# Kernel tuning notes

Hardware: AMD Instinct MI355X
Metric: run time of the kernel (lower is better)

The kernel has to match this reference:

```python
import jax, jax.numpy as jnp
import numpy as np

L = 3          # num_layers
D = 512        # hidden_dim
B, N = 8, 1024
EPS = 1e-5


def layernorm(x, gamma, beta):
    mu = jnp.mean(x, axis=-1, keepdims=True)
    var = jnp.var(x, axis=-1, keepdims=True)
    return (x - mu) * jax.lax.rsqrt(var + EPS) * gamma + beta


def setup_inputs() -> dict:
    key = jax.random.key(0)
    ks = jax.random.split(key, 12)
    s = 1.0 / np.sqrt(D)
    node_features = jax.random.normal(ks[0], (B, N, D), dtype=jnp.float32)
    adjacency_matrix = jax.random.randint(ks[1], (B, N, N), 0, 2, dtype=jnp.int32)
    return {
        "node_features": node_features,
        "adjacency_matrix": adjacency_matrix,
        # attn_linear: Linear(2D, 1) -> weight [2D], bias scalar, per layer
        "attn_w": jax.random.normal(ks[2], (L, 2 * D), dtype=jnp.float32) * (1.0 / np.sqrt(2 * D)),
        "attn_b": jax.random.normal(ks[3], (L,), dtype=jnp.float32) * 0.01,
        "W1": jax.random.normal(ks[4], (L, D, 4 * D), dtype=jnp.float32) * s,
        "b1": jnp.zeros((L, 4 * D), dtype=jnp.float32),
        "W2": jax.random.normal(ks[5], (L, 4 * D, D), dtype=jnp.float32) * (1.0 / np.sqrt(4 * D)),
        "b2": jnp.zeros((L, D), dtype=jnp.float32),
        "g1": jnp.ones((L, D), dtype=jnp.float32),
        "beta1": jnp.zeros((L, D), dtype=jnp.float32),
        "g2": jnp.ones((L, D), dtype=jnp.float32),
        "beta2": jnp.zeros((L, D), dtype=jnp.float32),
    }


def reference(node_features, adjacency_matrix, attn_w, attn_b, W1, b1, W2, b2, g1, beta1, g2, beta2):
    n = adjacency_matrix.shape[-1]
    # adjacency + self loops; mask of allowed edges
    mask = (adjacency_matrix.astype(jnp.float32) + jnp.eye(n, dtype=jnp.float32)) > 0  # [B,N,N]
    x = node_features
    d = x.shape[-1]
    for l in range(attn_w.shape[0]):
        # score_ij = a1.h_i + a2.h_j + b  (== Linear(concat(h_i,h_j)))
        si = x @ attn_w[l, :d]           # [B,N]
        sj = x @ attn_w[l, d:]           # [B,N]
        scores = si[:, :, None] + sj[:, None, :] + attn_b[l]   # [B,N,N]
        scores = jnp.where(scores >= 0, scores, 0.2 * scores)  # LeakyReLU(0.2)
        scores = jnp.where(mask, scores, -jnp.inf)
        attn = jax.nn.softmax(scores, axis=-1)                  # diag always unmasked
        agg = jnp.einsum('bij,bjd->bid', attn, x)
        h = layernorm(x + agg, g1[l], beta1[l])
        ff = jax.nn.gelu(h @ W1[l] + b1[l], approximate=False) @ W2[l] + b2[l]
        x = layernorm(h + ff, g2[l], beta2[l])
    return x
```

## Files before the change

### kernel.cpp

```cpp
#include <hip/hip_runtime.h>
#include <math.h>

#define NB 8
#define NN 1024
#define DD 512

typedef unsigned short u16;
typedef unsigned int u32;
typedef unsigned long long u64;
typedef __attribute__((ext_vector_type(8))) short bfrag;
typedef __attribute__((ext_vector_type(4))) float ffrag;

__device__ __forceinline__ u16 f2b(float f) {
    union { float f; u32 u; } v; v.f = f;
    u32 r = v.u + 0x7fffu + ((v.u >> 16) & 1u);
    return (u16)(r >> 16);
}
__device__ __forceinline__ float b2f(u16 b) {
    union { u32 u; float f; } v; v.u = ((u32)b) << 16;
    return v.f;
}

__device__ __forceinline__ float gelu_cheap(float v) {
    float s = v * 0.70710678118654752f;
    float a = fabsf(s);
    float t = 1.0f / (1.0f + 0.3275911f * a);
    float p = ((((1.061405429f * t - 1.453152027f) * t + 1.421413741f) * t
                - 0.284496736f) * t + 0.254829592f) * t;
    float erfa = 1.0f - p * __expf(-a * a);
    float erfs = copysignf(erfa, s);
    return 0.5f * v * (1.0f + erfs);
}

__device__ __forceinline__ void gload_lds16(const void* g, void* l) {
    __builtin_amdgcn_global_load_lds(
        (const __attribute__((address_space(1))) void*)g,
        (__attribute__((address_space(3))) void*)l, 16, 0, 0);
}

__global__ __launch_bounds__(256) void mask_pack(const int* __restrict__ adj,
                                                 u64* __restrict__ mb) {
    int idx = blockIdx.x * 256 + threadIdx.x;
    int w = idx & 15;
    int bi = idx >> 4;
    int i = bi & 1023;
    const int4* p = (const int4*)(adj + (size_t)bi * NN + w * 64);
    u64 m = 0;
#pragma unroll
    for (int q = 0; q < 16; ++q) {
        int4 v = p[q];
        if (v.x > 0) m |= 1ull << (q * 4 + 0);
        if (v.y > 0) m |= 1ull << (q * 4 + 1);
        if (v.z > 0) m |= 1ull << (q * 4 + 2);
        if (v.w > 0) m |= 1ull << (q * 4 + 3);
    }
    if (w == (i >> 6)) m |= 1ull << (i & 63);
    mb[idx] = m;
}

__global__ __launch_bounds__(256) void transpose_cvt(
    const float* __restrict__ in, u16* __restrict__ out,
    int R, int C, size_t inStr, size_t outStr)
{
    __shared__ float tile[32][33];
    int z = blockIdx.z;
    int r0 = blockIdx.y * 32, c0 = blockIdx.x * 32;
    int t = threadIdx.x;
    int tr = t >> 3, tc = (t & 7) * 4;
    float4 v = *(const float4*)(in + inStr * z + (size_t)(r0 + tr) * C + c0 + tc);
    tile[tr][tc + 0] = v.x; tile[tr][tc + 1] = v.y;
    tile[tr][tc + 2] = v.z; tile[tr][tc + 3] = v.w;
    __syncthreads();
    u32 w0 = (u32)f2b(tile[tc + 0][tr]) | ((u32)f2b(tile[tc + 1][tr]) << 16);
    u32 w1 = (u32)f2b(tile[tc + 2][tr]) | ((u32)f2b(tile[tc + 3][tr]) << 16);
    uint2 wv; wv.x = w0; wv.y = w1;
    *(uint2*)(out + outStr * z + (size_t)(c0 + tr) * R + r0 + tc) = wv;
}

__global__ __launch_bounds__(256) void score_proj_kernel(
    const float* __restrict__ x, const float* __restrict__ w,
    float* __restrict__ si, float* __restrict__ sj)
{
    int wave = threadIdx.x >> 6;
    int lane = threadIdx.x & 63;
    int row = blockIdx.x * 4 + wave;
    const float4* xr = (const float4*)(x + (size_t)row * DD) + lane * 2;
    const float4* w1 = (const float4*)(w) + lane * 2;
    const float4* w2 = (const float4*)(w + DD) + lane * 2;
    float a = 0.f, b2 = 0.f;
#pragma unroll
    for (int c = 0; c < 2; ++c) {
        float4 xv = xr[c], wa = w1[c], wb = w2[c];
        a  += xv.x * wa.x + xv.y * wa.y + xv.z * wa.z + xv.w * wa.w;
        b2 += xv.x * wb.x + xv.y * wb.y + xv.z * wb.z + xv.w * wb.w;
    }
#pragma unroll
    for (int off = 32; off > 0; off >>= 1) {
        a  += __shfl_xor(a, off);
        b2 += __shfl_xor(b2, off);
    }
    if (lane == 0) { si[row] = a; sj[row] = b2; }
}

__global__ __launch_bounds__(256) void softmax_p(
    const float* __restrict__ si, const float* __restrict__ sj,
    const float* __restrict__ attn_b, const u64* __restrict__ mb,
    u16* __restrict__ P)
{
    __shared__ u16 sb[8 * NN];
    int b  = blockIdx.x >> 7;
    int i0 = (blockIdx.x & 127) * 8;
    int tid = threadIdx.x;
    int r = tid >> 5, l32 = tid & 31;
    int i = i0 + r;
    float bb = attn_b[0];
    float siv = si[b * NN + i];
    const float* sjb = sj + b * NN;
    const u64* mbr = mb + ((size_t)b * NN + i) * 16;

    float sv[32];
    float mx = -INFINITY;
#pragma unroll
    for (int q = 0; q < 32; ++q) {
        int j = q * 32 + l32;
        u64 w = mbr[q >> 1];
        int bit = ((q & 1) << 5) + l32;
        float s = siv + sjb[j] + bb;
        s = (s >= 0.f) ? s : 0.2f * s;
        s = ((w >> bit) & 1ull) ? s : -INFINITY;
        sv[q] = s;
        mx = fmaxf(mx, s);
    }
#pragma unroll
    for (int off = 16; off > 0; off >>= 1) mx = fmaxf(mx, __shfl_xor(mx, off, 32));
    float sum = 0.f;
#pragma unroll
    for (int q = 0; q < 32; ++q) {
        float p = __expf(sv[q] - mx);
        sv[q] = p;
        sum += p;
    }
#pragma unroll
    for (int off = 16; off > 0; off >>= 1) sum += __shfl_xor(sum, off, 32);
    float inv = 1.f / sum;
#pragma unroll
    for (int q = 0; q < 32; ++q)
        sb[r * NN + q * 32 + l32] = f2b(sv[q] * inv);
    __syncthreads();
    const uint4* src = (const uint4*)sb;
    uint4* dst = (uint4*)(P + ((size_t)b * NN + i0) * NN);
#pragma unroll
    for (int t = 0; t < 4; ++t) dst[t * 256 + tid] = src[t * 256 + tid];
}

template <int EPI>
__global__ __launch_bounds__(256) void gemm64(
    const u16* __restrict__ A, const u16* __restrict__ Bm,
    const float* __restrict__ bias, const void* __restrict__ res,
    void* __restrict__ Cout, int K, int N, int lda, int ldb,
    size_t aStr, size_t bStr, size_t cStr, size_t resStr)
{
    __shared__ __align__(16) u16 lds[24576];
    int z = blockIdx.z;
    int m0 = blockIdx.y * 64, n0 = blockIdx.x * 128;
    int tid = threadIdx.x;
    int lane = tid & 63, wv = tid >> 6;

    const u16* ag[2]; const u16* bg[4];
    u32 la[2], lb[4];
#pragma unroll
    for (int i = 0; i < 2; ++i) {
        int q = i * 256 + tid;
        int row = q >> 3, c = q & 7;
        ag[i] = A + aStr * z + (size_t)(m0 + row) * lda + (c ^ (row & 7)) * 8;
        la[i] = i * 2048 + wv * 512;
    }
#pragma unroll
    for (int i = 0; i < 4; ++i) {
        int q = i * 256 + tid;
        int row = q >> 3, c = q & 7;
        bg[i] = Bm + bStr * z + (size_t)(n0 + row) * ldb + (c ^ (row & 7)) * 8;
        lb[i] = 8192 + i * 2048 + wv * 512;
    }

    int mw = (wv >> 1) * 32, nw = (wv & 1) * 64;
    int lr = lane & 15, lq = lane >> 4;
    int sw = lr & 7;

    ffrag acc[2][4];
#pragma unroll
    for (int i = 0; i < 2; ++i)
#pragma unroll
        for (int j = 0; j < 4; ++j) acc[i][j] = (ffrag){0.f, 0.f, 0.f, 0.f};

#pragma unroll
    for (int i = 0; i < 2; ++i) gload_lds16(ag[i], &lds[la[i]]);
#pragma unroll
    for (int i = 0; i < 4; ++i) gload_lds16(bg[i], &lds[lb[i]]);

    for (int k0 = 0; k0 < K; k0 += 64) {
        int cur = (k0 >> 6) & 1;
        if (k0 + 64 < K) {
#pragma unroll
            for (int i = 0; i < 2; ++i)
                gload_lds16(ag[i] + k0 + 64, &lds[((cur ^ 1) << 12) + la[i]]);
#pragma unroll
            for (int i = 0; i < 4; ++i)
                gload_lds16(bg[i] + k0 + 64, &lds[((cur ^ 1) << 13) + lb[i]]);
            asm volatile("s_waitcnt vmcnt(6)" ::: "memory");
        } else {
            asm volatile("s_waitcnt vmcnt(0)" ::: "memory");
        }
        asm volatile("s_barrier" ::: "memory");

        const u16* Ab = &lds[cur << 12];
        const u16* Bb = &lds[8192 + (cur << 13)];
#pragma unroll
        for (int h = 0; h < 2; ++h) {
            bfrag af[2], bf[4];
#pragma unroll
            for (int i = 0; i < 2; ++i)
                af[i] = *(const bfrag*)&Ab[(mw + i * 16 + lr) * 64 + ((h * 4 + lq) ^ sw) * 8];
#pragma unroll
            for (int j = 0; j < 4; ++j)
                bf[j] = *(const bfrag*)&Bb[(nw + j * 16 + lr) * 64 + ((h * 4 + lq) ^ sw) * 8];
#pragma unroll
            for (int i = 0; i < 2; ++i)
#pragma unroll
                for (int j = 0; j < 4; ++j)
                    acc[i][j] = __builtin_amdgcn_mfma_f32_16x16x32_bf16(af[i], bf[j], acc[i][j], 0, 0, 0);
        }
        asm volatile("s_waitcnt lgkmcnt(0)\ns_barrier" ::: "memory");
    }

    float* Cf = (float*)Cout + cStr * z;
    u16*   Cb = (u16*)Cout + cStr * z;
    const float* resf = (const float*)res;
    const u16*   resb = (const u16*)res;
#pragma unroll
    for (int i = 0; i < 2; ++i) {
        int row = m0 + mw + i * 16 + lq * 4;
#pragma unroll
        for (int j = 0; j < 4; ++j) {
            int col = n0 + nw + j * 16 + lr;
            float bv = (EPI != 0) ? bias[col] : 0.f;
#pragma unroll
            for (int r = 0; r < 4; ++r) {
                float v = acc[i][j][r] + bv;
                size_t off = (size_t)(row + r) * N + col;
                if (EPI == 1) {
                    Cb[off] = f2b(gelu_cheap(v));
                } else if (EPI == 0) {
                    Cf[off] = v + resf[resStr * z + off];
                } else {
                    Cf[off] = v + b2f(resb[off]);
                }
            }
        }
    }
}

template <bool BF>
__global__ __launch_bounds__(256) void ln_kernel(
    const float* __restrict__ in, const float* __restrict__ g,
    const float* __restrict__ be, void* __restrict__ out)
{
    int row = blockIdx.x;
    int tid = threadIdx.x;
    const float2* rp = (const float2*)(in + (size_t)row * DD);
    float2 v = rp[tid];
    float s  = v.x + v.y;
    float ss = v.x * v.x + v.y * v.y;
#pragma unroll
    for (int off = 32; off > 0; off >>= 1) {
        s  += __shfl_xor(s, off);
        ss += __shfl_xor(ss, off);
    }
    __shared__ float sh[8];
    int wave = tid >> 6, lane = tid & 63;
    if (lane == 0) { sh[wave] = s; sh[4 + wave] = ss; }
    __syncthreads();
    float S  = sh[0] + sh[1] + sh[2] + sh[3];
    float SS = sh[4] + sh[5] + sh[6] + sh[7];
    float mean = S * (1.f / DD);
    float var  = SS * (1.f / DD) - mean * mean;
    var = fmaxf(var, 0.f);
    float rs = rsqrtf(var + 1e-5f);
    float2 gv = ((const float2*)g)[tid];
    float2 bv = ((const float2*)be)[tid];
    float ox = (v.x - mean) * rs * gv.x + bv.x;
    float oy = (v.y - mean) * rs * gv.y + bv.y;
    if (BF) {
        u32 w = (u32)f2b(ox) | ((u32)f2b(oy) << 16);
        ((u32*)out)[(size_t)row * (DD / 2) + tid] = w;
    } else {
        float2 o; o.x = ox; o.y = oy;
        ((float2*)out)[(size_t)row * (DD / 2) + tid] = o;
    }
}

extern "C" void kernel_launch(void* const* d_in, const int* in_sizes, int n_in,
                              void* d_out, int out_size, void* d_ws, size_t ws_size,
                              hipStream_t stream) {
    const float* nf     = (const float*)d_in[0];
    const int*   adj    = (const int*)d_in[1];
    const float* attn_w = (const float*)d_in[2];
    const float* attn_b = (const float*)d_in[3];
    const float* W1     = (const float*)d_in[4];
    const float* b1     = (const float*)d_in[5];
    const float* W2     = (const float*)d_in[6];
    const float* b2     = (const float*)d_in[7];
    const float* g1     = (const float*)d_in[8];
    const float* be1    = (const float*)d_in[9];
    const float* g2     = (const float*)d_in[10];
    const float* be2    = (const float*)d_in[11];
    float* out = (float*)d_out;

    char* wsb = (char*)d_ws;
    float* x_cur = (float*)(wsb);
    u16*   h_bf  = (u16*)(wsb + 16777216);
    char*  scr   = wsb + 25165824;
    u16*   P     = (u16*)scr;
    float* hres  = (float*)(scr + 16777216);
    u16*   mid   = (u16*)scr;
    u16*   xT    = (u16*)(wsb + 58720256);
    u16*   W1t   = (u16*)(wsb + 67108864);
    u16*   W2t   = (u16*)(wsb + 73400320);
    u64*   mask  = (u64*)(wsb + 79691776);
    float* si    = (float*)(wsb + 80740352);
    float* sj    = (float*)(wsb + 80773120);

    mask_pack<<<512, 256, 0, stream>>>(adj, mask);
    transpose_cvt<<<dim3(64, 16, 3), 256, 0, stream>>>(W1, W1t, 512, 2048,
                                                       (size_t)512 * 2048, (size_t)512 * 2048);
    transpose_cvt<<<dim3(16, 64, 3), 256, 0, stream>>>(W2, W2t, 2048, 512,
                                                       (size_t)2048 * 512, (size_t)2048 * 512);

    for (int l = 0; l < 3; ++l) {
        const float* xin = (l == 0) ? nf : x_cur;
        score_proj_kernel<<<2048, 256, 0, stream>>>(xin, attn_w + (size_t)l * 1024, si, sj);
        transpose_cvt<<<dim3(16, 32, 8), 256, 0, stream>>>(xin, xT, 1024, 512,
                                                           (size_t)NN * DD, (size_t)NN * DD);
        softmax_p<<<1024, 256, 0, stream>>>(si, sj, attn_b + l, mask, P);
        gemm64<0><<<dim3(4, 16, 8), 256, 0, stream>>>(
            P, xT, nullptr, xin, hres, 1024, 512, 1024, 1024,
            (size_t)NN * NN, (size_t)DD * NN, (size_t)NN * DD, (size_t)NN * DD);
        ln_kernel<true><<<8192, 256, 0, stream>>>(hres, g1 + (size_t)l * 512, be1 + (size_t)l * 512, h_bf);
        gemm64<1><<<dim3(16, 128, 1), 256, 0, stream>>>(
            h_bf, W1t + (size_t)l * 1048576, b1 + (size_t)l * 2048, nullptr, mid,
            512, 2048, 512, 512, 0, 0, 0, 0);
        gemm64<2><<<dim3(4, 128, 1), 256, 0, stream>>>(
            mid, W2t + (size_t)l * 1048576, b2 + (size_t)l * 512, h_bf, x_cur,
            2048, 512, 2048, 2048, 0, 0, 0, 0);
        void* lnout = (l == 2) ? (void*)out : (void*)x_cur;
        ln_kernel<false><<<8192, 256, 0, stream>>>(x_cur, g2 + (size_t)l * 512, be2 + (size_t)l * 512, lnout);
    }
}
```

Baseline: 474.9 us.

## Use 128x128 tiled GEMM for FFN up-projection and fuse score projection into LayerNorm

Adds a gemm128 kernel with 128x128 output tiles, double-buffered LDS and XOR-swizzled loads, and uses it for the W1 GELU GEMM in place of the 64-tile version. This is meant to raise data reuse per loaded tile. Separately, the attention score projections (si, sj) for the next layer are now computed inside the second LayerNorm kernel, which removes a separate pass over x for layers 1 and 2. The trade-offs are a larger register and LDS footprint for the GEMM and an extra reduction plus barriers in the LN kernel.

After: 476.0 us. Within noise of the previous version (+0.2%).

```diff
diff --git a/kernel.cpp b/kernel.cpp
--- a/kernel.cpp
+++ b/kernel.cpp
@@ -260,10 +260,113 @@
     }
 }
 
-template <bool BF>
+template <int EPI>
+__global__ __launch_bounds__(256) void gemm128(
+    const u16* __restrict__ A, const u16* __restrict__ Bm,
+    const float* __restrict__ bias, const void* __restrict__ res,
+    void* __restrict__ Cout, int K, int N, int lda, int ldb,
+    size_t aStr, size_t bStr, size_t cStr, size_t resStr)
+{
+    __shared__ __align__(16) u16 lds[32768];
+    int z = blockIdx.z;
+    int m0 = blockIdx.y * 128, n0 = blockIdx.x * 128;
+    int tid = threadIdx.x;
+    int lane = tid & 63, wv = tid >> 6;
+
+    const u16* ag[4]; const u16* bg[4];
+    u32 la[4], lb[4];
+#pragma unroll
+    for (int i = 0; i < 4; ++i) {
+        int q = i * 256 + tid;
+        int row = q >> 3, c = q & 7;
+        ag[i] = A + aStr * z + (size_t)(m0 + row) * lda + (c ^ (row & 7)) * 8;
+        la[i] = i * 2048 + wv * 512;
+        bg[i] = Bm + bStr * z + (size_t)(n0 + row) * ldb + (c ^ (row & 7)) * 8;
+        lb[i] = 16384 + i * 2048 + wv * 512;
+    }
+
+    int mw = (wv >> 1) * 64, nw = (wv & 1) * 64;
+    int lr = lane & 15, lq = lane >> 4;
+    int sw = lr & 7;
+
+    ffrag acc[4][4];
+#pragma unroll
+    for (int i = 0; i < 4; ++i)
+#pragma unroll
+        for (int j = 0; j < 4; ++j) acc[i][j] = (ffrag){0.f, 0.f, 0.f, 0.f};
+
+#pragma unroll
+    for (int i = 0; i < 4; ++i) gload_lds16(ag[i], &lds[la[i]]);
+#pragma unroll
+    for (int i = 0; i < 4; ++i) gload_lds16(bg[i], &lds[lb[i]]);
+
+    for (int k0 = 0; k0 < K; k0 += 64) {
+        int cur = (k0 >> 6) & 1;
+        if (k0 + 64 < K) {
+#pragma unroll
+            for (int i = 0; i < 4; ++i)
+                gload_lds16(ag[i] + k0 + 64, &lds[((cur ^ 1) << 13) + la[i]]);
+#pragma unroll
+            for (int i = 0; i < 4; ++i)
+                gload_lds16(bg[i] + k0 + 64, &lds[((cur ^ 1) << 13) + lb[i]]);
+            asm volatile("s_waitcnt vmcnt(8)" ::: "memory");
+        } else {
+            asm volatile("s_waitcnt vmcnt(0)" ::: "memory");
+        }
+        asm volatile("s_barrier" ::: "memory");
+
+        const u16* Ab = &lds[cur << 13];
+        const u16* Bb = &lds[16384 + (cur << 13)];
+#pragma unroll
+        for (int h = 0; h < 2; ++h) {
+            bfrag af[4], bf[4];
+#pragma unroll
+            for (int i = 0; i < 4; ++i)
+                af[i] = *(const bfrag*)&Ab[(mw + i * 16 + lr) * 64 + ((h * 4 + lq) ^ sw) * 8];
+#pragma unroll
+            for (int j = 0; j < 4; ++j)
+                bf[j] = *(const bfrag*)&Bb[(nw + j * 16 + lr) * 64 + ((h * 4 + lq) ^ sw) * 8];
+#pragma unroll
+            for (int i = 0; i < 4; ++i)
+#pragma unroll
+                for (int j = 0; j < 4; ++j)
+                    acc[i][j] = __builtin_amdgcn_mfma_f32_16x16x32_bf16(af[i], bf[j], acc[i][j], 0, 0, 0);
+        }
+        asm volatile("s_waitcnt lgkmcnt(0)\ns_barrier" ::: "memory");
+    }
+
+    float* Cf = (float*)Cout + cStr * z;
+    u16*   Cb = (u16*)Cout + cStr * z;
+    const float* resf = (const float*)res;
+    const u16*   resb = (const u16*)res;
+#pragma unroll
+    for (int i = 0; i < 4; ++i) {
+        int row = m0 + mw + i * 16 + lq * 4;
+#pragma unroll
+        for (int j = 0; j < 4; ++j) {
+            int col = n0 + nw + j * 16 + lr;
+            float bv = (EPI != 0) ? bias[col] : 0.f;
+#pragma unroll
+            for (int r = 0; r < 4; ++r) {
+                float v = acc[i][j][r] + bv;
+                size_t off = (size_t)(row + r) * N + col;
+                if (EPI == 1) {
+                    Cb[off] = f2b(gelu_cheap(v));
+                } else if (EPI == 0) {
+                    Cf[off] = v + resf[resStr * z + off];
+                } else {
+                    Cf[off] = v + b2f(resb[off]);
+                }
+            }
+        }
+    }
+}
+
+template <bool BF, bool SP>
 __global__ __launch_bounds__(256) void ln_kernel(
     const float* __restrict__ in, const float* __restrict__ g,
-    const float* __restrict__ be, void* __restrict__ out)
+    const float* __restrict__ be, void* __restrict__ out,
+    const float* __restrict__ aw, float* __restrict__ si, float* __restrict__ sj)
 {
     int row = blockIdx.x;
     int tid = threadIdx.x;
@@ -297,6 +400,24 @@
         float2 o; o.x = ox; o.y = oy;
         ((float2*)out)[(size_t)row * (DD / 2) + tid] = o;
     }
+    if (SP) {
+        float2 wa = ((const float2*)aw)[tid];
+        float2 wb = ((const float2*)(aw + DD))[tid];
+        float a = ox * wa.x + oy * wa.y;
+        float c = ox * wb.x + oy * wb.y;
+#pragma unroll
+        for (int off = 32; off > 0; off >>= 1) {
+            a += __shfl_xor(a, off);
+            c += __shfl_xor(c, off);
+        }
+        __syncthreads();
+        if (lane == 0) { sh[wave] = a; sh[4 + wave] = c; }
+        __syncthreads();
+        if (tid == 0) {
+            si[row] = sh[0] + sh[1] + sh[2] + sh[3];
+            sj[row] = sh[4] + sh[5] + sh[6] + sh[7];
+        }
+    }
 }
 
 extern "C" void kernel_launch(void* const* d_in, const int* in_sizes, int n_in,
@@ -336,23 +457,32 @@
     transpose_cvt<<<dim3(16, 64, 3), 256, 0, stream>>>(W2, W2t, 2048, 512,
                                                        (size_t)2048 * 512, (size_t)2048 * 512);
 
+    score_proj_kernel<<<2048, 256, 0, stream>>>(nf, attn_w, si, sj);
+
     for (int l = 0; l < 3; ++l) {
         const float* xin = (l == 0) ? nf : x_cur;
-        score_proj_kernel<<<2048, 256, 0, stream>>>(xin, attn_w + (size_t)l * 1024, si, sj);
         transpose_cvt<<<dim3(16, 32, 8), 256, 0, stream>>>(xin, xT, 1024, 512,
                                                            (size_t)NN * DD, (size_t)NN * DD);
         softmax_p<<<1024, 256, 0, stream>>>(si, sj, attn_b + l, mask, P);
         gemm64<0><<<dim3(4, 16, 8), 256, 0, stream>>>(
             P, xT, nullptr, xin, hres, 1024, 512, 1024, 1024,
             (size_t)NN * NN, (size_t)DD * NN, (size_t)NN * DD, (size_t)NN * DD);
-        ln_kernel<true><<<8192, 256, 0, stream>>>(hres, g1 + (size_t)l * 512, be1 + (size_t)l * 512, h_bf);
-        gemm64<1><<<dim3(16, 128, 1), 256, 0, stream>>>(
+        ln_kernel<true, false><<<8192, 256, 0, stream>>>(
+            hres, g1 + (size_t)l * 512, be1 + (size_t)l * 512, h_bf, nullptr, nullptr, nullptr);
+        gemm128<1><<<dim3(16, 64, 1), 256, 0, stream>>>(
             h_bf, W1t + (size_t)l * 1048576, b1 + (size_t)l * 2048, nullptr, mid,
             512, 2048, 512, 512, 0, 0, 0, 0);
         gemm64<2><<<dim3(4, 128, 1), 256, 0, stream>>>(
             mid, W2t + (size_t)l * 1048576, b2 + (size_t)l * 512, h_bf, x_cur,
             2048, 512, 2048, 2048, 0, 0, 0, 0);
-        void* lnout = (l == 2) ? (void*)out : (void*)x_cur;
-        ln_kernel<false><<<8192, 256, 0, stream>>>(x_cur, g2 + (size_t)l * 512, be2 + (size_t)l * 512, lnout);
-    }
-}
+        if (l < 2) {
+            ln_kernel<false, true><<<8192, 256, 0, stream>>>(
+                x_cur, g2 + (size_t)l * 512, be2 + (size_t)l * 512, x_cur,
+                attn_w + (size_t)(l + 1) * 1024, si, sj);
+        } else {
+            ln_kernel<false, false><<<8192, 256, 0, stream>>>(
+                x_cur, g2 + (size_t)l * 512, be2 + (size_t)l * 512, out,
+                nullptr, nullptr, nullptr);
+        }
+    }
+}
```
